# Kernel optimization log

Hardware: AMD Instinct MI355X
Metric: run time of the kernel (lower is better)

Reference implementation:

```python
import jax, jax.numpy as jnp
import numpy as np

MODEL_DIM = 1024
N_HEADS = 16
HEAD_DIM = 64  # q_dim == k_dim == v_dim


def setup_inputs() -> dict:
    key = jax.random.key(0)
    ks = jax.random.split(key, 7)
    B, S = 4, 2048
    scale = 1.0 / np.sqrt(MODEL_DIM)
    return {
        "q": jax.random.normal(ks[0], (B, S, MODEL_DIM), dtype=jnp.float32),
        "k": jax.random.normal(ks[1], (B, S, MODEL_DIM), dtype=jnp.float32),
        "v": jax.random.normal(ks[2], (B, S, MODEL_DIM), dtype=jnp.float32),
        # Linear weights stored as [out, in] like torch; no biases.
        "wq": jax.random.normal(ks[3], (N_HEADS * HEAD_DIM, MODEL_DIM), dtype=jnp.float32) * scale,
        "wk": jax.random.normal(ks[4], (N_HEADS * HEAD_DIM, MODEL_DIM), dtype=jnp.float32) * scale,
        "wv": jax.random.normal(ks[5], (N_HEADS * HEAD_DIM, MODEL_DIM), dtype=jnp.float32) * scale,
        "wo": jax.random.normal(ks[6], (MODEL_DIM, N_HEADS * HEAD_DIM), dtype=jnp.float32) * scale,
    }


def reference(q, k, v, wq, wk, wv, wo):
    B, Sq, _ = q.shape
    Sk = k.shape[1]
    # projections: [B,S,D] @ W^T -> [B,S,H*dh] -> [B,H,S,dh]
    qh = (q @ wq.T).reshape(B, Sq, N_HEADS, HEAD_DIM).transpose(0, 2, 1, 3)
    kh = (k @ wk.T).reshape(B, Sk, N_HEADS, HEAD_DIM).transpose(0, 2, 1, 3)
    vh = (v @ wv.T).reshape(B, Sk, N_HEADS, HEAD_DIM).transpose(0, 2, 1, 3)
    # scores [B,H,Sq,Sk], scaled by sqrt(k_dim)
    scores = jnp.einsum('bhqd,bhkd->bhqk', qh, kh) / jnp.sqrt(jnp.float32(HEAD_DIM))
    attn = jax.nn.softmax(scores, axis=-1)
    ctx = jnp.einsum('bhqk,bhkd->bhqd', attn, vh)  # [B,H,Sq,dh]
    ctx = ctx.transpose(0, 2, 1, 3).reshape(B, Sq, N_HEADS * HEAD_DIM)
    return ctx @ wo.T
```

## Files before the change

kernel.cpp:

```cpp
#include <hip/hip_runtime.h>
#include <cstdint>
#include <cstddef>


typedef _Float16 f16x8 __attribute__((ext_vector_type(8)));
typedef _Float16 f16x4 __attribute__((ext_vector_type(4)));
typedef _Float16 f16x2 __attribute__((ext_vector_type(2)));
typedef __fp16 h16x2 __attribute__((ext_vector_type(2)));
typedef float f32x4 __attribute__((ext_vector_type(4)));

#define LDS_CAST(p) ((__attribute__((address_space(3))) void*)(p))
#define GLB_CAST(p) ((const __attribute__((address_space(1))) void*)(p))

__device__ __forceinline__ void gload_lds16(const void* g, void* l) {
  __builtin_amdgcn_global_load_lds(GLB_CAST(g), LDS_CAST(l), 16, 0, 0);
}

__device__ __forceinline__ float fexp2(float x) {
#if __has_builtin(__builtin_amdgcn_exp2f)
  return __builtin_amdgcn_exp2f(x);
#else
  return exp2f(x);
#endif
}

__device__ __forceinline__ f16x2 pkrtz(float a, float b) {
  h16x2 r = __builtin_amdgcn_cvt_pkrtz(a, b);
  return __builtin_bit_cast(f16x2, r);
}

__device__ __forceinline__ float dot2acc(f16x2 a, float acc) {
#if __has_builtin(__builtin_amdgcn_fdot2)
  const f16x2 one2 = {(_Float16)1.0f, (_Float16)1.0f};
  return __builtin_amdgcn_fdot2(a, one2, acc, false);
#else
  return acc + (float)a[0] + (float)a[1];
#endif
}

__global__ void cvt3_kernel(const float* __restrict__ a,
                            const float* __restrict__ b,
                            const float* __restrict__ c,
                            _Float16* __restrict__ oa, _Float16* __restrict__ ob,
                            _Float16* __restrict__ oc) {
  const float* in = blockIdx.z == 0 ? a : blockIdx.z == 1 ? b : c;
  _Float16* out = blockIdx.z == 0 ? oa : blockIdx.z == 1 ? ob : oc;
  int i = blockIdx.x * 256 + threadIdx.x;
  float4 v = ((const float4*)in)[i];
  f16x4 o = {(_Float16)v.x, (_Float16)v.y, (_Float16)v.z, (_Float16)v.w};
  ((f16x4*)out)[i] = o;
}

__global__ void cvt4_kernel(const float* __restrict__ a,
                            const float* __restrict__ b,
                            const float* __restrict__ c,
                            const float* __restrict__ d,
                            _Float16* __restrict__ oa, _Float16* __restrict__ ob,
                            _Float16* __restrict__ oc, _Float16* __restrict__ od) {
  int z = blockIdx.z;
  const float* in = z == 0 ? a : z == 1 ? b : z == 2 ? c : d;
  _Float16* out = z == 0 ? oa : z == 1 ? ob : z == 2 ? oc : od;
  int i = blockIdx.x * 256 + threadIdx.x;
  float4 v = ((const float4*)in)[i];
  f16x4 o = {(_Float16)v.x, (_Float16)v.y, (_Float16)v.z, (_Float16)v.w};
  ((f16x4*)out)[i] = o;
}

template <int MODE>
__device__ __forceinline__ void gemm_core(const _Float16* __restrict__ A,
                                          const _Float16* __restrict__ W,
                                          void* __restrict__ C, float scale,
                                          _Float16* As, _Float16* Bs) {
  constexpr int K = 1024, N = 1024;
  const int tid = threadIdx.x;
  const int wid = tid >> 6;
  const int lane = tid & 63;
  const int quad = lane >> 4;
  const int l16 = lane & 15;
  const int wm = wid >> 1;
  const int wn = wid & 1;
  const int m0 = blockIdx.y * 128;
  const int n0 = blockIdx.x * 128;

  const _Float16* Ag = A + (size_t)m0 * K;
  const _Float16* Bg = W + (size_t)n0 * K;

  f32x4 acc[4][4];
#pragma unroll
  for (int i = 0; i < 4; i++)
#pragma unroll
    for (int j = 0; j < 4; j++) acc[i][j] = (f32x4){0.f, 0.f, 0.f, 0.f};

  const int lrow = lane >> 2;
  const int lcol = (lane & 3) * 8;

  for (int k0 = 0; k0 < K; k0 += 32) {
#pragma unroll
    for (int i = 0; i < 2; i++) {
      int issue = wid * 2 + i;
      gload_lds16(Ag + (size_t)(issue * 16 + lrow) * K + k0 + lcol,
                  &As[issue * 512]);
      gload_lds16(Bg + (size_t)(issue * 16 + lrow) * K + k0 + lcol,
                  &Bs[issue * 512]);
    }
    __syncthreads();
    f16x8 af[4], bfr[4];
#pragma unroll
    for (int mt = 0; mt < 4; mt++)
      af[mt] = *(const f16x8*)&As[(wm * 64 + mt * 16 + l16) * 32 + quad * 8];
#pragma unroll
    for (int nt = 0; nt < 4; nt++)
      bfr[nt] = *(const f16x8*)&Bs[(wn * 64 + nt * 16 + l16) * 32 + quad * 8];
#pragma unroll
    for (int mt = 0; mt < 4; mt++)
#pragma unroll
      for (int nt = 0; nt < 4; nt++)
        acc[mt][nt] = __builtin_amdgcn_mfma_f32_16x16x32_f16(
            af[mt], bfr[nt], acc[mt][nt], 0, 0, 0);
    __syncthreads();
  }

#pragma unroll
  for (int mt = 0; mt < 4; mt++) {
#pragma unroll
    for (int nt = 0; nt < 4; nt++) {
#pragma unroll
      for (int r = 0; r < 4; r++) {
        int m = m0 + wm * 64 + mt * 16 + quad * 4 + r;
        int n = n0 + wn * 64 + nt * 16 + l16;
        float v = acc[mt][nt][r] * scale;
        if (MODE == 0) {
          ((float*)C)[(size_t)m * N + n] = v;
        } else {
          int b = m >> 11, s = m & 2047;
          int h = n >> 6, dd = n & 63;
          size_t bh = (size_t)(b * 16 + h);
          if (MODE == 1) {
            ((_Float16*)C)[(bh * 2048 + s) * 64 + dd] = (_Float16)v;
          } else if (MODE == 3) {
            int kt = s >> 6, ntk = (s >> 4) & 3, lk = s & 15;
            int hh = dd >> 5, qk = (dd >> 3) & 3, j = dd & 7;
            size_t idx =
                (((bh * 32 + kt) * 4 + ntk) * 64 + qk * 16 + lk) * 16 + hh * 8 + j;
            ((_Float16*)C)[idx] = (_Float16)v;
          } else {
            int kt = s >> 6, k16 = (s >> 4) & 3, qv = (s >> 2) & 3, jk = s & 3;
            int dt = dd >> 4, lv = dd & 15;
            size_t idx =
                (((bh * 32 + kt) * 4 + dt) * 64 + qv * 16 + lv) * 16 + k16 * 4 + jk;
            ((_Float16*)C)[idx] = (_Float16)v;
          }
        }
      }
    }
  }
}

__global__ __launch_bounds__(256) void gemm_qkv(
    const _Float16* __restrict__ qb, const _Float16* __restrict__ kb,
    const _Float16* __restrict__ vb, const _Float16* __restrict__ wq,
    const _Float16* __restrict__ wk, const _Float16* __restrict__ wv,
    _Float16* __restrict__ Qh, _Float16* __restrict__ Kf,
    _Float16* __restrict__ Vf) {
  __shared__ _Float16 As[128 * 32];
  __shared__ _Float16 Bs[128 * 32];
  if (blockIdx.z == 0)
    gemm_core<1>(qb, wq, Qh, 0.18033688f, As, Bs);
  else if (blockIdx.z == 1)
    gemm_core<3>(kb, wk, Kf, 1.0f, As, Bs);
  else
    gemm_core<4>(vb, wv, Vf, 1.0f, As, Bs);
}

__global__ __launch_bounds__(256) void gemm_wo(const _Float16* __restrict__ ctx,
                                               const _Float16* __restrict__ wo,
                                               float* __restrict__ out) {
  __shared__ _Float16 As[128 * 32];
  __shared__ _Float16 Bs[128 * 32];
  gemm_core<0>(ctx, wo, out, 1.0f, As, Bs);
}

__global__ __launch_bounds__(256, 4) void attn_kernel(
    const _Float16* __restrict__ Qh, const _Float16* __restrict__ Kf,
    const _Float16* __restrict__ Vf, _Float16* __restrict__ ctx) {
  const int qt = blockIdx.x;
  const int bh = blockIdx.y;
  const int tid = threadIdx.x;
  const int wid = tid >> 6;
  const int lane = tid & 63;
  const int quad = lane >> 4;
  const int l16 = lane & 15;

  const _Float16* Qg = Qh + ((size_t)bh * 2048 + qt * 128 + wid * 32) * 64;
  const _Float16* Kb = Kf + (size_t)bh * 131072;
  const _Float16* Vb = Vf + (size_t)bh * 131072;

  f16x8 aq[2][2];
#pragma unroll
  for (int mt = 0; mt < 2; mt++)
#pragma unroll
    for (int h = 0; h < 2; h++)
      aq[mt][h] =
          *(const f16x8*)(Qg + (size_t)(mt * 16 + l16) * 64 + h * 32 + quad * 8);

  f32x4 acc[4][2];
#pragma unroll
  for (int dt = 0; dt < 4; dt++)
#pragma unroll
    for (int mt = 0; mt < 2; mt++) acc[dt][mt] = (f32x4){0.f, 0.f, 0.f, 0.f};
  float lsum[2] = {0.f, 0.f};

  for (int kt = 0; kt < 32; kt++) {
    const _Float16* Kt = Kb + kt * 4096;
    const _Float16* Vt = Vb + kt * 4096;

    f16x8 kfrag[4][2];
#pragma unroll
    for (int nt = 0; nt < 4; nt++) {
      const _Float16* p = Kt + nt * 1024 + lane * 16;
      kfrag[nt][0] = *(const f16x8*)p;
      kfrag[nt][1] = *(const f16x8*)(p + 8);
    }
    f16x8 vreg[4][2];
#pragma unroll
    for (int dt = 0; dt < 4; dt++) {
      const _Float16* p = Vt + dt * 1024 + lane * 16;
      vreg[dt][0] = *(const f16x8*)p;
      vreg[dt][1] = *(const f16x8*)(p + 8);
    }

    f32x4 st[2][4];
#pragma unroll
    for (int mt = 0; mt < 2; mt++)
#pragma unroll
      for (int nt = 0; nt < 4; nt++) {
        f32x4 z = (f32x4){0.f, 0.f, 0.f, 0.f};
        z = __builtin_amdgcn_mfma_f32_16x16x32_f16(kfrag[nt][0], aq[mt][0], z,
                                                   0, 0, 0);
        z = __builtin_amdgcn_mfma_f32_16x16x32_f16(kfrag[nt][1], aq[mt][1], z,
                                                   0, 0, 0);
        st[mt][nt] = z;
      }

    f16x4 pb[2][4];
#pragma unroll
    for (int mt = 0; mt < 2; mt++) {
#pragma unroll
      for (int nt = 0; nt < 4; nt++) {
        float p0 = fexp2(st[mt][nt][0]);
        float p1 = fexp2(st[mt][nt][1]);
        float p2 = fexp2(st[mt][nt][2]);
        float p3 = fexp2(st[mt][nt][3]);
        f16x2 h01 = pkrtz(p0, p1);
        f16x2 h23 = pkrtz(p2, p3);
        lsum[mt] = dot2acc(h01, lsum[mt]);
        lsum[mt] = dot2acc(h23, lsum[mt]);
        pb[mt][nt] = __builtin_shufflevector(h01, h23, 0, 1, 2, 3);
      }
    }

#pragma unroll
    for (int dt = 0; dt < 4; dt++) {
      f16x4 vs[4];
      vs[0] = __builtin_shufflevector(vreg[dt][0], vreg[dt][0], 0, 1, 2, 3);
      vs[1] = __builtin_shufflevector(vreg[dt][0], vreg[dt][0], 4, 5, 6, 7);
      vs[2] = __builtin_shufflevector(vreg[dt][1], vreg[dt][1], 0, 1, 2, 3);
      vs[3] = __builtin_shufflevector(vreg[dt][1], vreg[dt][1], 4, 5, 6, 7);
#pragma unroll
      for (int nt = 0; nt < 4; nt++)
#pragma unroll
        for (int mt = 0; mt < 2; mt++)
          acc[dt][mt] = __builtin_amdgcn_mfma_f32_16x16x16f16(
              vs[nt], pb[mt][nt], acc[dt][mt], 0, 0, 0);
    }
  }

  const int b = bh >> 4, h = bh & 15;
#pragma unroll
  for (int mt = 0; mt < 2; mt++) {
    float l = lsum[mt];
    l += __shfl_xor(l, 16);
    l += __shfl_xor(l, 32);
    float inv = 1.f / l;
    int s = qt * 128 + wid * 32 + mt * 16 + l16;
#pragma unroll
    for (int dt = 0; dt < 4; dt++) {
      f16x4 o;
#pragma unroll
      for (int r = 0; r < 4; r++) o[r] = (_Float16)(acc[dt][mt][r] * inv);
      *(f16x4*)(ctx + ((size_t)b * 2048 + s) * 1024 + h * 64 + dt * 16 +
                quad * 4) = o;
    }
  }
}

extern "C" void kernel_launch(void* const* d_in, const int* in_sizes, int n_in,
                              void* d_out, int out_size, void* d_ws,
                              size_t ws_size, hipStream_t stream) {
  const float* q = (const float*)d_in[0];
  const float* k = (const float*)d_in[1];
  const float* v = (const float*)d_in[2];
  const float* wq = (const float*)d_in[3];
  const float* wk = (const float*)d_in[4];
  const float* wv = (const float*)d_in[5];
  const float* wo = (const float*)d_in[6];
  float* out = (float*)d_out;

  const size_t SD = (size_t)8192 * 1024;
  const size_t WSZ = (size_t)1024 * 1024;

  _Float16* ws = (_Float16*)d_ws;
  _Float16* qb = ws;
  _Float16* kb = ws + 1 * SD;
  _Float16* vb = ws + 2 * SD;
  _Float16* Qh = ws + 3 * SD;
  _Float16* Kf = ws + 4 * SD;
  _Float16* Vf = ws + 5 * SD;
  _Float16* ctx = ws + 6 * SD;
  _Float16* wqb = ws + 7 * SD;
  _Float16* wkb = wqb + WSZ;
  _Float16* wvb = wqb + 2 * WSZ;
  _Float16* wob = wqb + 3 * WSZ;

  cvt3_kernel<<<dim3(8192, 1, 3), 256, 0, stream>>>(q, k, v, qb, kb, vb);
  cvt4_kernel<<<dim3(1024, 1, 4), 256, 0, stream>>>(wq, wk, wv, wo, wqb, wkb,
                                                    wvb, wob);

  gemm_qkv<<<dim3(8, 64, 3), 256, 0, stream>>>(qb, kb, vb, wqb, wkb, wvb, Qh,
                                               Kf, Vf);

  attn_kernel<<<dim3(16, 64), 256, 0, stream>>>(Qh, Kf, Vf, ctx);

  gemm_wo<<<dim3(8, 64), 256, 0, stream>>>(ctx, wob, out);
}
```

Before: 349.3 us.

## Prefetch next K/V tile in attention, narrow output GEMM tiles, merge conversion kernels

The attention loop now loads the next K tile after the score MFMAs and the next V tile after the PV MFMAs, so global loads overlap compute instead of stalling at the start of each iteration. The output projection GEMM uses a 128x64 tile, doubling the block count for better CU occupancy at the cost of reloading A tiles more often. The two fp32-to-fp16 conversion launches are merged into one, adding many early-exit blocks for the weight slices. The prefetch raises register pressure, which may affect occupancy.

```diff
diff --git a/kernel.cpp b/kernel.cpp
--- a/kernel.cpp
+++ b/kernel.cpp
@@ -38,40 +38,39 @@
 #endif
 }
 
-__global__ void cvt3_kernel(const float* __restrict__ a,
-                            const float* __restrict__ b,
-                            const float* __restrict__ c,
-                            _Float16* __restrict__ oa, _Float16* __restrict__ ob,
-                            _Float16* __restrict__ oc) {
-  const float* in = blockIdx.z == 0 ? a : blockIdx.z == 1 ? b : c;
-  _Float16* out = blockIdx.z == 0 ? oa : blockIdx.z == 1 ? ob : oc;
+__global__ void cvt_all(const float* __restrict__ q, const float* __restrict__ k,
+                        const float* __restrict__ v, const float* __restrict__ wq,
+                        const float* __restrict__ wk, const float* __restrict__ wv,
+                        const float* __restrict__ wo, _Float16* __restrict__ oq,
+                        _Float16* __restrict__ ok, _Float16* __restrict__ ov,
+                        _Float16* __restrict__ owq, _Float16* __restrict__ owk,
+                        _Float16* __restrict__ owv, _Float16* __restrict__ owo) {
+  int z = blockIdx.z;
+  if (z >= 3 && blockIdx.x >= 1024) return;
+  const float* in;
+  _Float16* out;
+  switch (z) {
+    case 0: in = q; out = oq; break;
+    case 1: in = k; out = ok; break;
+    case 2: in = v; out = ov; break;
+    case 3: in = wq; out = owq; break;
+    case 4: in = wk; out = owk; break;
+    case 5: in = wv; out = owv; break;
+    default: in = wo; out = owo; break;
+  }
   int i = blockIdx.x * 256 + threadIdx.x;
-  float4 v = ((const float4*)in)[i];
-  f16x4 o = {(_Float16)v.x, (_Float16)v.y, (_Float16)v.z, (_Float16)v.w};
+  float4 val = ((const float4*)in)[i];
+  f16x4 o = {(_Float16)val.x, (_Float16)val.y, (_Float16)val.z, (_Float16)val.w};
   ((f16x4*)out)[i] = o;
 }
 
-__global__ void cvt4_kernel(const float* __restrict__ a,
-                            const float* __restrict__ b,
-                            const float* __restrict__ c,
-                            const float* __restrict__ d,
-                            _Float16* __restrict__ oa, _Float16* __restrict__ ob,
-                            _Float16* __restrict__ oc, _Float16* __restrict__ od) {
-  int z = blockIdx.z;
-  const float* in = z == 0 ? a : z == 1 ? b : z == 2 ? c : d;
-  _Float16* out = z == 0 ? oa : z == 1 ? ob : z == 2 ? oc : od;
-  int i = blockIdx.x * 256 + threadIdx.x;
-  float4 v = ((const float4*)in)[i];
-  f16x4 o = {(_Float16)v.x, (_Float16)v.y, (_Float16)v.z, (_Float16)v.w};
-  ((f16x4*)out)[i] = o;
-}
-
-template <int MODE>
+template <int MODE, int TN>
 __device__ __forceinline__ void gemm_core(const _Float16* __restrict__ A,
                                           const _Float16* __restrict__ W,
                                           void* __restrict__ C, float scale,
                                           _Float16* As, _Float16* Bs) {
   constexpr int K = 1024, N = 1024;
+  constexpr int NTW = TN / 32;
   const int tid = threadIdx.x;
   const int wid = tid >> 6;
   const int lane = tid & 63;
@@ -80,41 +79,43 @@
   const int wm = wid >> 1;
   const int wn = wid & 1;
   const int m0 = blockIdx.y * 128;
-  const int n0 = blockIdx.x * 128;
+  const int n0 = blockIdx.x * TN;
 
   const _Float16* Ag = A + (size_t)m0 * K;
   const _Float16* Bg = W + (size_t)n0 * K;
 
-  f32x4 acc[4][4];
+  f32x4 acc[4][NTW];
 #pragma unroll
   for (int i = 0; i < 4; i++)
 #pragma unroll
-    for (int j = 0; j < 4; j++) acc[i][j] = (f32x4){0.f, 0.f, 0.f, 0.f};
-
-  const int lrow = lane >> 2;
-  const int lcol = (lane & 3) * 8;
+    for (int j = 0; j < NTW; j++) acc[i][j] = (f32x4){0.f, 0.f, 0.f, 0.f};
 
   for (int k0 = 0; k0 < K; k0 += 32) {
 #pragma unroll
     for (int i = 0; i < 2; i++) {
-      int issue = wid * 2 + i;
-      gload_lds16(Ag + (size_t)(issue * 16 + lrow) * K + k0 + lcol,
-                  &As[issue * 512]);
-      gload_lds16(Bg + (size_t)(issue * 16 + lrow) * K + k0 + lcol,
-                  &Bs[issue * 512]);
+      int c = (wid * 2 + i) * 64 + lane;
+      gload_lds16(Ag + (size_t)(c >> 2) * K + k0 + (c & 3) * 8,
+                  &As[(size_t)(c >> 2) * 32 + (c & 3) * 8]);
+    }
+#pragma unroll
+    for (int i = 0; i < TN / 64; i++) {
+      int c = (wid * (TN / 64) + i) * 64 + lane;
+      gload_lds16(Bg + (size_t)(c >> 2) * K + k0 + (c & 3) * 8,
+                  &Bs[(size_t)(c >> 2) * 32 + (c & 3) * 8]);
     }
     __syncthreads();
-    f16x8 af[4], bfr[4];
+    f16x8 af[4], bfr[NTW];
 #pragma unroll
     for (int mt = 0; mt < 4; mt++)
       af[mt] = *(const f16x8*)&As[(wm * 64 + mt * 16 + l16) * 32 + quad * 8];
 #pragma unroll
-    for (int nt = 0; nt < 4; nt++)
-      bfr[nt] = *(const f16x8*)&Bs[(wn * 64 + nt * 16 + l16) * 32 + quad * 8];
+    for (int nt = 0; nt < NTW; nt++)
+      bfr[nt] =
+          *(const f16x8*)&Bs[(wn * (TN / 2) + nt * 16 + l16) * 32 + quad * 8];
 #pragma unroll
     for (int mt = 0; mt < 4; mt++)
 #pragma unroll
-      for (int nt = 0; nt < 4; nt++)
+      for (int nt = 0; nt < NTW; nt++)
         acc[mt][nt] = __builtin_amdgcn_mfma_f32_16x16x32_f16(
             af[mt], bfr[nt], acc[mt][nt], 0, 0, 0);
     __syncthreads();
@@ -123,11 +124,11 @@
 #pragma unroll
   for (int mt = 0; mt < 4; mt++) {
 #pragma unroll
-    for (int nt = 0; nt < 4; nt++) {
+    for (int nt = 0; nt < NTW; nt++) {
 #pragma unroll
       for (int r = 0; r < 4; r++) {
         int m = m0 + wm * 64 + mt * 16 + quad * 4 + r;
-        int n = n0 + wn * 64 + nt * 16 + l16;
+        int n = n0 + wn * (TN / 2) + nt * 16 + l16;
         float v = acc[mt][nt][r] * scale;
         if (MODE == 0) {
           ((float*)C)[(size_t)m * N + n] = v;
@@ -165,19 +166,19 @@
   __shared__ _Float16 As[128 * 32];
   __shared__ _Float16 Bs[128 * 32];
   if (blockIdx.z == 0)
-    gemm_core<1>(qb, wq, Qh, 0.18033688f, As, Bs);
+    gemm_core<1, 128>(qb, wq, Qh, 0.18033688f, As, Bs);
   else if (blockIdx.z == 1)
-    gemm_core<3>(kb, wk, Kf, 1.0f, As, Bs);
+    gemm_core<3, 128>(kb, wk, Kf, 1.0f, As, Bs);
   else
-    gemm_core<4>(vb, wv, Vf, 1.0f, As, Bs);
+    gemm_core<4, 128>(vb, wv, Vf, 1.0f, As, Bs);
 }
 
 __global__ __launch_bounds__(256) void gemm_wo(const _Float16* __restrict__ ctx,
                                                const _Float16* __restrict__ wo,
                                                float* __restrict__ out) {
   __shared__ _Float16 As[128 * 32];
-  __shared__ _Float16 Bs[128 * 32];
-  gemm_core<0>(ctx, wo, out, 1.0f, As, Bs);
+  __shared__ _Float16 Bs[64 * 32];
+  gemm_core<0, 64>(ctx, wo, out, 1.0f, As, Bs);
 }
 
 __global__ __launch_bounds__(256, 4) void attn_kernel(
@@ -210,25 +211,23 @@
     for (int mt = 0; mt < 2; mt++) acc[dt][mt] = (f32x4){0.f, 0.f, 0.f, 0.f};
   float lsum[2] = {0.f, 0.f};
 
+  f16x8 kfrag[4][2];
+  f16x8 vreg[4][2];
+
+#pragma unroll
+  for (int nt = 0; nt < 4; nt++) {
+    const _Float16* p = Kb + nt * 1024 + lane * 16;
+    kfrag[nt][0] = *(const f16x8*)p;
+    kfrag[nt][1] = *(const f16x8*)(p + 8);
+  }
+#pragma unroll
+  for (int dt = 0; dt < 4; dt++) {
+    const _Float16* p = Vb + dt * 1024 + lane * 16;
+    vreg[dt][0] = *(const f16x8*)p;
+    vreg[dt][1] = *(const f16x8*)(p + 8);
+  }
+
   for (int kt = 0; kt < 32; kt++) {
-    const _Float16* Kt = Kb + kt * 4096;
-    const _Float16* Vt = Vb + kt * 4096;
-
-    f16x8 kfrag[4][2];
-#pragma unroll
-    for (int nt = 0; nt < 4; nt++) {
-      const _Float16* p = Kt + nt * 1024 + lane * 16;
-      kfrag[nt][0] = *(const f16x8*)p;
-      kfrag[nt][1] = *(const f16x8*)(p + 8);
-    }
-    f16x8 vreg[4][2];
-#pragma unroll
-    for (int dt = 0; dt < 4; dt++) {
-      const _Float16* p = Vt + dt * 1024 + lane * 16;
-      vreg[dt][0] = *(const f16x8*)p;
-      vreg[dt][1] = *(const f16x8*)(p + 8);
-    }
-
     f32x4 st[2][4];
 #pragma unroll
     for (int mt = 0; mt < 2; mt++)
@@ -241,6 +240,16 @@
                                                    0, 0, 0);
         st[mt][nt] = z;
       }
+
+    if (kt < 31) {
+      const _Float16* Kt = Kb + (kt + 1) * 4096;
+#pragma unroll
+      for (int nt = 0; nt < 4; nt++) {
+        const _Float16* p = Kt + nt * 1024 + lane * 16;
+        kfrag[nt][0] = *(const f16x8*)p;
+        kfrag[nt][1] = *(const f16x8*)(p + 8);
+      }
+    }
 
     f16x4 pb[2][4];
 #pragma unroll
@@ -272,6 +281,16 @@
         for (int mt = 0; mt < 2; mt++)
           acc[dt][mt] = __builtin_amdgcn_mfma_f32_16x16x16f16(
               vs[nt], pb[mt][nt], acc[dt][mt], 0, 0, 0);
+    }
+
+    if (kt < 31) {
+      const _Float16* Vt = Vb + (kt + 1) * 4096;
+#pragma unroll
+      for (int dt = 0; dt < 4; dt++) {
+        const _Float16* p = Vt + dt * 1024 + lane * 16;
+        vreg[dt][0] = *(const f16x8*)p;
+        vreg[dt][1] = *(const f16x8*)(p + 8);
+      }
     }
   }
 
@@ -322,14 +341,13 @@
   _Float16* wvb = wqb + 2 * WSZ;
   _Float16* wob = wqb + 3 * WSZ;
 
-  cvt3_kernel<<<dim3(8192, 1, 3), 256, 0, stream>>>(q, k, v, qb, kb, vb);
-  cvt4_kernel<<<dim3(1024, 1, 4), 256, 0, stream>>>(wq, wk, wv, wo, wqb, wkb,
-                                                    wvb, wob);
+  cvt_all<<<dim3(8192, 1, 7), 256, 0, stream>>>(q, k, v, wq, wk, wv, wo, qb,
+                                                kb, vb, wqb, wkb, wvb, wob);
 
   gemm_qkv<<<dim3(8, 64, 3), 256, 0, stream>>>(qb, kb, vb, wqb, wkb, wvb, Qh,
                                                Kf, Vf);
 
   attn_kernel<<<dim3(16, 64), 256, 0, stream>>>(Qh, Kf, Vf, ctx);
 
-  gemm_wo<<<dim3(8, 64), 256, 0, stream>>>(ctx, wob, out);
-}
+  gemm_wo<<<dim3(16, 64), 256, 0, stream>>>(ctx, wob, out);
+}
```

New measurement: 377.4 us. +8.1%, slower.
